# Performance work log

Measured on AMD Instinct MI355X. Metric: run time of the kernel, lower is better.

The kernel has to match this reference:

```python
import jax, jax.numpy as jnp
import numpy as np

N_HEADS = 16
ROPE_BASE = 10000.0

def apply_rope(x):
    # x: [B, H, S, D] with D even; interleaved-pair RoPE (torchtune style)
    B, H, S, D = x.shape
    half = D // 2
    inv_freq = 1.0 / (ROPE_BASE ** (jnp.arange(0, half, dtype=jnp.float32) / half))
    angles = jnp.arange(S, dtype=jnp.float32)[:, None] * inv_freq[None, :]  # [S, D/2]
    cos = jnp.cos(angles)[None, None]  # [1,1,S,D/2]
    sin = jnp.sin(angles)[None, None]
    x1 = x[..., 0::2]
    x2 = x[..., 1::2]
    r1 = x1 * cos - x2 * sin
    r2 = x1 * sin + x2 * cos
    return jnp.stack([r1, r2], axis=-1).reshape(B, H, S, D)

def setup_inputs() -> dict:
    key = jax.random.key(0)
    ks = jax.random.split(key, 5)
    B, S, E = 2, 2048, 1024
    d_attn = 1024
    scale = 1.0 / np.sqrt(E)
    x = jax.random.normal(ks[0], (B, S, E), dtype=jnp.float32)
    Wq = jax.random.normal(ks[1], (d_attn, E), dtype=jnp.float32) * scale
    Wk = jax.random.normal(ks[2], (d_attn, E), dtype=jnp.float32) * scale
    Wv = jax.random.normal(ks[3], (d_attn, E), dtype=jnp.float32) * scale
    Wo = jax.random.normal(ks[4], (E, d_attn), dtype=jnp.float32) * scale
    return {"x": x, "Wq": Wq, "Wk": Wk, "Wv": Wv, "Wo": Wo}

def reference(x, Wq, Wk, Wv, Wo):
    B, S, E = x.shape
    d_attn = Wq.shape[0]
    hd = d_attn // N_HEADS
    attn_scale = 1.0 / np.sqrt(d_attn)
    # projections (nn.Linear: x @ W.T), split heads -> [B, H, S, hd]
    q = (x @ Wq.T).reshape(B, S, N_HEADS, hd).transpose(0, 2, 1, 3)
    k = (x @ Wk.T).reshape(B, S, N_HEADS, hd).transpose(0, 2, 1, 3)
    v = (x @ Wv.T).reshape(B, S, N_HEADS, hd).transpose(0, 2, 1, 3)
    q = apply_rope(q)
    k = apply_rope(k)
    scores = jnp.einsum('bhqd,bhkd->bhqk', q, k) * attn_scale  # [B,H,S,S]
    causal = jnp.tril(jnp.ones((S, S), dtype=bool))
    scores = jnp.where(causal[None, None], scores, -jnp.inf)
    probs = jax.nn.softmax(scores, axis=-1)  # dropout is identity in eval
    out = jnp.einsum('bhqk,bhkd->bhqd', probs, v)
    out = out.transpose(0, 2, 1, 3).reshape(B, S, d_attn)
    return out @ Wo.T
```

## Files before the change

kernel.cpp:

```cpp
#include <hip/hip_runtime.h>


typedef float  f32x4  __attribute__((ext_vector_type(4)));
typedef short  short8 __attribute__((ext_vector_type(8)));

#define MFMA16(a,b,c) __builtin_amdgcn_mfma_f32_16x16x32_bf16((a),(b),(c),0,0,0)
#define GLD_LDS16(g, l)                                                        \
  __builtin_amdgcn_global_load_lds(                                            \
      (const __attribute__((address_space(1))) unsigned int*)(g),              \
      (__attribute__((address_space(3))) unsigned int*)(l), 16, 0, 0)

__device__ __forceinline__ unsigned short f2bf(float f) {
  unsigned int x = __float_as_uint(f);
  x += 0x7fffu + ((x >> 16) & 1u);
  return (unsigned short)(x >> 16);
}
__device__ __forceinline__ float bf2f(unsigned short u) {
  return __uint_as_float(((unsigned int)u) << 16);
}
__device__ __forceinline__ unsigned int cvtpk_bf16(float lo, float hi) {
  unsigned int r;
  asm("v_cvt_pk_bf16_f32 %0, %1, %2" : "=v"(r) : "v"(lo), "v"(hi));
  return r;
}

__global__ __launch_bounds__(256) void cvt_all(const float* __restrict__ x,
                                               const float* __restrict__ wq,
                                               const float* __restrict__ wk,
                                               const float* __restrict__ wv,
                                               const float* __restrict__ wo,
                                               ushort* __restrict__ dst) {
  const int i = blockIdx.x * 256 + threadIdx.x;
  const float* src;
  int off;
  if (i < 1048576) { src = x; off = i; }
  else {
    const int j = i - 1048576;
    const int wsel = j >> 18;
    off = j & 262143;
    src = (wsel == 0) ? wq : (wsel == 1) ? wk : (wsel == 2) ? wv : wo;
  }
  const float4 v = ((const float4*)src)[off];
  ushort4 o = make_ushort4(f2bf(v.x), f2bf(v.y), f2bf(v.z), f2bf(v.w));
  ((ushort4*)dst)[i] = o;
}

template<int MODE, int BN, int BM>
__global__ __launch_bounds__(256) void gemm_bt(const ushort* __restrict__ A,
                                               const ushort* __restrict__ B,
                                               void* __restrict__ Cv,
                                               int K) {
  constexpr int NI = BN / 32;
  constexpr int MI = BM / 32;
  constexpr int AI = BM / 64;
  constexpr int BI = BN / 64;
  __shared__ __align__(16) short As0[BM * 32];
  __shared__ __align__(16) short As1[BM * 32];
  __shared__ __align__(16) short Bs0[BN * 32];
  __shared__ __align__(16) short Bs1[BN * 32];
  const int tid  = threadIdx.x;
  const int lane = tid & 63, w = tid >> 6;
  const int ln   = lane & 15, quad = lane >> 4;
  const int wm   = w >> 1, wn = w & 1;
  const int m0 = blockIdx.y * BM, n0 = blockIdx.x * BN;

  const int srow = lane >> 2;
  const int schk = (lane & 3) * 8;
  const int arow = w * (16 * AI);
  const int brow = w * (16 * BI);
  const ushort* Ag0 = A + (size_t)(m0 + arow + srow) * K + schk;
  const ushort* Ag1 = A + (size_t)(m0 + arow + 16 + srow) * K + schk;
  const ushort* Bg0 = B + (size_t)(n0 + brow + srow) * K + schk;
  const ushort* Bg1 = B + (size_t)(n0 + brow + 16 + srow) * K + schk;
  const int lA0 = arow * 32, lA1 = (arow + 16) * 32;
  const int lB0 = brow * 32, lB1 = (brow + 16) * 32;

  int aoff[MI], boff[NI];
#pragma unroll
  for (int i = 0; i < MI; i++)
    aoff[i] = (wm * (BM / 2) + i * 16 + ln) * 32 + quad * 8;
#pragma unroll
  for (int i = 0; i < NI; i++)
    boff[i] = (wn * (BN / 2) + i * 16 + ln) * 32 + quad * 8;
  f32x4 acc[MI][NI] = {};

  for (int kt = 0; kt < K; kt += 64) {
    __syncthreads();
    GLD_LDS16(Ag0 + kt, As0 + lA0);
    if (AI == 2) GLD_LDS16(Ag1 + kt, As0 + lA1);
    GLD_LDS16(Ag0 + kt + 32, As1 + lA0);
    if (AI == 2) GLD_LDS16(Ag1 + kt + 32, As1 + lA1);
    GLD_LDS16(Bg0 + kt, Bs0 + lB0);
    if (BI == 2) GLD_LDS16(Bg1 + kt, Bs0 + lB1);
    GLD_LDS16(Bg0 + kt + 32, Bs1 + lB0);
    if (BI == 2) GLD_LDS16(Bg1 + kt + 32, Bs1 + lB1);
    __syncthreads();
#pragma unroll
    for (int h = 0; h < 2; ++h) {
      const short* Ap = h ? As1 : As0;
      const short* Bp = h ? Bs1 : Bs0;
      short8 av[MI], bv[NI];
#pragma unroll
      for (int i = 0; i < MI; i++) av[i] = *(const short8*)&Ap[aoff[i]];
#pragma unroll
      for (int i = 0; i < NI; i++) bv[i] = *(const short8*)&Bp[boff[i]];
#pragma unroll
      for (int mi = 0; mi < MI; mi++)
#pragma unroll
        for (int ni = 0; ni < NI; ni++)
          acc[mi][ni] = MFMA16(av[mi], bv[ni], acc[mi][ni]);
    }
  }

  if (MODE == 0) {
    ushort* Cq = (ushort*)Cv;
    if (n0 < 2048) {
      ushort* dst = Cq + (n0 < 1024 ? 0 : 4194304);
      const int nbase = (n0 < 1024) ? n0 : n0 - 1024;
      const float qsc = (n0 < 1024) ? 0.04508422002778011f : 1.0f;
      const float sgn = (ln & 1) ? 1.0f : -1.0f;
      float invc[NI];
#pragma unroll
      for (int ni = 0; ni < NI; ni++) {
        const int ii = ((wn * (BN / 2) + ni * 16 + ln) & 63) >> 1;
        invc[ni] = __builtin_amdgcn_exp2f(-(float)ii * 0.4152410118579865f) *
                   0.15915494309189535f;
      }
#pragma unroll
      for (int mi = 0; mi < MI; mi++) {
        const int row = m0 + wm * (BM / 2) + mi * 16 + quad * 4;
#pragma unroll
        for (int ni = 0; ni < NI; ni++) {
          const int col = nbase + wn * (BN / 2) + ni * 16 + ln;
#pragma unroll
          for (int r = 0; r < 4; r++) {
            const float mine  = acc[mi][ni][r];
            const float other = __shfl_xor(mine, 1, 64);
            const int   s     = (row + r) & 2047;
            const float rev   = (float)s * invc[ni];
            const float rr    = rev - floorf(rev);
            const float sn = __builtin_amdgcn_sinf(rr);
            const float cs = __builtin_amdgcn_cosf(rr);
            const float rot = (mine * cs + sgn * other * sn) * qsc;
            dst[(size_t)(row + r) * 1024 + col] = f2bf(rot);
          }
        }
      }
    } else {
      ushort* vt = Cq + 8388608;
#pragma unroll
      for (int mi = 0; mi < MI; mi++) {
        const int sm = m0 + wm * (BM / 2) + mi * 16 + quad * 4;
        const int b = sm >> 11, s = sm & 2047;
#pragma unroll
        for (int ni = 0; ni < NI; ni++) {
          const int nv = (n0 - 2048) + wn * (BN / 2) + ni * 16 + ln;
          const int bh = b * 16 + (nv >> 6), d = nv & 63;
          ushort4 u = make_ushort4(f2bf(acc[mi][ni][0]), f2bf(acc[mi][ni][1]),
                                   f2bf(acc[mi][ni][2]), f2bf(acc[mi][ni][3]));
          *(ushort4*)&vt[((size_t)bh * 64 + d) * 2048 + s] = u;
        }
      }
    }
  } else {
    float* C = (float*)Cv;
#pragma unroll
    for (int mi = 0; mi < MI; mi++) {
      const int row = m0 + wm * (BM / 2) + mi * 16 + quad * 4;
#pragma unroll
      for (int ni = 0; ni < NI; ni++) {
        const int col = n0 + wn * (BN / 2) + ni * 16 + ln;
#pragma unroll
        for (int r = 0; r < 4; r++)
          C[(size_t)(row + r) * 1024 + col] = acc[mi][ni][r];
      }
    }
  }
}

__global__ __launch_bounds__(512) void attnk(const ushort* __restrict__ q,
                                             const ushort* __restrict__ k,
                                             const ushort* __restrict__ vt,
                                             ushort* __restrict__ ctx) {
  __shared__ __align__(16) short Ks[2][64 * 72];
  __shared__ __align__(16) short Vs[2][64 * 72];
  __shared__ __align__(16) short Ps[8 * 16 * 72];
  const int tid  = threadIdx.x;
  const int lane = tid & 63, w = tid >> 6;
  const int ln   = lane & 15, quad = lane >> 4;
  const int x = blockIdx.x, bh = blockIdx.y;
  const int b = bh >> 4, h = bh & 15;
  const int jA = x, jB = 31 - x;
  const int tile = w >> 2;
  const int wq   = w & 3;
  const int j    = tile ? jA : jB;
  short* Pw = Ps + w * 1152;

  const size_t qb = ((size_t)(b * 2048 + j * 64 + wq * 16 + ln)) * 1024 + h * 64;
  const short8 aq0 = *(const short8*)&q[qb + quad * 8];
  const short8 aq1 = *(const short8*)&q[qb + 32 + quad * 8];

  f32x4 o[4] = {};
  float ls0 = 0.f, ls1 = 0.f;

  const int r0 = tid >> 3, c0 = (tid & 7) * 8;
  const ushort* kg = k  + ((size_t)(b * 2048 + r0)) * 1024 + h * 64 + c0;
  const ushort* vg = vt + ((size_t)(bh * 64 + r0)) * 2048 + c0;
  const int wK = r0 * 72 + c0;

  short8 kr = *(const short8*)(kg);
  short8 vr = *(const short8*)(vg);
  *(short8*)&Ks[0][wK] = kr;
  *(short8*)&Vs[0][wK] = vr;
  kr = *(const short8*)(kg + 65536);
  vr = *(const short8*)(vg + 64);

  const int qloc = j * 64 + wq * 16 + ln;

  for (int t = 0; t <= jB; t++) {
    __syncthreads();
    const short* Kc = Ks[t & 1];
    const short* Vc = Vs[t & 1];
    if (t < jB) {
      *(short8*)&Ks[(t & 1) ^ 1][wK] = kr;
      *(short8*)&Vs[(t & 1) ^ 1][wK] = vr;
    }
    if (t + 2 <= jB) {
      kr = *(const short8*)(kg + (size_t)(t + 2) * 65536);
      vr = *(const short8*)(vg + (t + 2) * 64);
    }

    const bool act = (tile == 0) || (t <= jA);
    if (act) {
      f32x4 sc[4];
#pragma unroll
      for (int ct = 0; ct < 4; ct++) {
        const short8 bk0 = *(const short8*)&Kc[(ct * 16 + ln) * 72 + quad * 8];
        const short8 bk1 = *(const short8*)&Kc[(ct * 16 + ln) * 72 + 32 + quad * 8];
        f32x4 z = {0.f, 0.f, 0.f, 0.f};
        z = MFMA16(bk0, aq0, z);
        z = MFMA16(bk1, aq1, z);
        sc[ct] = z;
      }
      if (t == j) {
#pragma unroll
        for (int ct = 0; ct < 4; ct++) {
          const int kvb = (t << 6) + ct * 16 + quad * 4;
#pragma unroll
          for (int r = 0; r < 4; r++)
            if (kvb + r > qloc) sc[ct][r] = -100000.0f;
        }
      }

      short8 bv0[4], bv1[4];
#pragma unroll
      for (int dt = 0; dt < 4; dt++) {
        bv0[dt] = *(const short8*)&Vc[(dt * 16 + ln) * 72 + quad * 8];
        bv1[dt] = *(const short8*)&Vc[(dt * 16 + ln) * 72 + 32 + quad * 8];
      }

#pragma unroll
      for (int ct = 0; ct < 4; ct++) {
        const float p0 = __builtin_amdgcn_exp2f(sc[ct][0]);
        const float p1 = __builtin_amdgcn_exp2f(sc[ct][1]);
        const float p2 = __builtin_amdgcn_exp2f(sc[ct][2]);
        const float p3 = __builtin_amdgcn_exp2f(sc[ct][3]);
        ls0 += p0 + p1;
        ls1 += p2 + p3;
        const uint2 u = make_uint2(cvtpk_bf16(p0, p1), cvtpk_bf16(p2, p3));
        *(uint2*)&Pw[ln * 72 + ct * 16 + quad * 4] = u;
      }
      const short8 ap0 = *(const short8*)&Pw[ln * 72 + quad * 8];
      const short8 ap1 = *(const short8*)&Pw[ln * 72 + 32 + quad * 8];
#pragma unroll
      for (int dt = 0; dt < 4; dt++) {
        o[dt] = MFMA16(ap0, bv0[dt], o[dt]);
        o[dt] = MFMA16(ap1, bv1[dt], o[dt]);
      }
    }
  }

  float l = ls0 + ls1;
  l += __shfl_xor(l, 16, 64);
  l += __shfl_xor(l, 32, 64);

#pragma unroll
  for (int r = 0; r < 4; r++) {
    const float inv = 1.0f / __shfl(l, quad * 4 + r, 64);
    const int row = j * 64 + wq * 16 + quad * 4 + r;
#pragma unroll
    for (int dt = 0; dt < 4; dt++) {
      ctx[((size_t)(b * 2048 + row)) * 1024 + h * 64 + dt * 16 + ln] =
          f2bf(o[dt][r] * inv);
    }
  }
}

extern "C" void kernel_launch(void* const* d_in, const int* in_sizes, int n_in,
                              void* d_out, int out_size, void* d_ws, size_t ws_size,
                              hipStream_t stream) {
  const float* x  = (const float*)d_in[0];
  const float* Wq = (const float*)d_in[1];
  const float* Wk = (const float*)d_in[2];
  const float* Wv = (const float*)d_in[3];
  const float* Wo = (const float*)d_in[4];
  float* out = (float*)d_out;
  char* ws = (char*)d_ws;

  ushort* xb  = (ushort*)(ws);
  ushort* wqb = (ushort*)(ws + (size_t)(8  << 20));
  ushort* qb  = (ushort*)(ws + (size_t)(16 << 20));
  ushort* kb  = (ushort*)(ws + (size_t)(24 << 20));
  ushort* vtb = (ushort*)(ws + (size_t)(32 << 20));
  ushort* ctx = (ushort*)(ws + (size_t)(40 << 20));

  cvt_all<<<8192, 256, 0, stream>>>(x, Wq, Wk, Wv, Wo, xb);
  gemm_bt<0, 64, 128><<<dim3(48, 32), 256, 0, stream>>>(xb, wqb, (void*)qb, 1024);
  attnk<<<dim3(16, 32), 512, 0, stream>>>(qb, kb, vtb, ctx);
  gemm_bt<2, 64, 64><<<dim3(16, 64), 256, 0, stream>>>(ctx, wqb + 3145728 , (void*)out, 1024);
}
```

Measured before the change: 175.1 us.

## Split attention KV tiles across wave groups instead of query tiles for balance

Previously the two wave groups each handled one of the paired query tiles (jA, jB), so the jA group went idle once its shorter causal range ended. Now both groups work on both query tiles and split each 64-key KV tile in half (32 keys each). Partial outputs and row sums are combined through shared memory at the end. This keeps all waves busy for the whole loop, at the cost of a final reduction, extra barriers and more registers for two accumulator sets.

```diff
diff --git a/kernel.cpp b/kernel.cpp
--- a/kernel.cpp
+++ b/kernel.cpp
@@ -184,24 +184,29 @@
                                              ushort* __restrict__ ctx) {
   __shared__ __align__(16) short Ks[2][64 * 72];
   __shared__ __align__(16) short Vs[2][64 * 72];
-  __shared__ __align__(16) short Ps[8 * 16 * 72];
+  __shared__ __align__(16) short PsB[8][16 * 48];
+  __shared__ __align__(16) short PsA[8][16 * 48];
   const int tid  = threadIdx.x;
   const int lane = tid & 63, w = tid >> 6;
   const int ln   = lane & 15, quad = lane >> 4;
   const int x = blockIdx.x, bh = blockIdx.y;
   const int b = bh >> 4, h = bh & 15;
   const int jA = x, jB = 31 - x;
-  const int tile = w >> 2;
+  const int g    = w >> 2;
   const int wq   = w & 3;
-  const int j    = tile ? jA : jB;
-  short* Pw = Ps + w * 1152;
-
-  const size_t qb = ((size_t)(b * 2048 + j * 64 + wq * 16 + ln)) * 1024 + h * 64;
-  const short8 aq0 = *(const short8*)&q[qb + quad * 8];
-  const short8 aq1 = *(const short8*)&q[qb + 32 + quad * 8];
-
-  f32x4 o[4] = {};
-  float ls0 = 0.f, ls1 = 0.f;
+  const int koff = g * 32;
+  short* PwB = PsB[w];
+  short* PwA = PsA[w];
+
+  const size_t qbA = ((size_t)(b * 2048 + jA * 64 + wq * 16 + ln)) * 1024 + h * 64;
+  const size_t qbB = ((size_t)(b * 2048 + jB * 64 + wq * 16 + ln)) * 1024 + h * 64;
+  const short8 aqA0 = *(const short8*)&q[qbA + quad * 8];
+  const short8 aqA1 = *(const short8*)&q[qbA + 32 + quad * 8];
+  const short8 aqB0 = *(const short8*)&q[qbB + quad * 8];
+  const short8 aqB1 = *(const short8*)&q[qbB + 32 + quad * 8];
+
+  f32x4 oA[4] = {}, oB[4] = {};
+  float lsA0 = 0.f, lsA1 = 0.f, lsB0 = 0.f, lsB1 = 0.f;
 
   const int r0 = tid >> 3, c0 = (tid & 7) * 8;
   const ushort* kg = k  + ((size_t)(b * 2048 + r0)) * 1024 + h * 64 + c0;
@@ -215,7 +220,8 @@
   kr = *(const short8*)(kg + 65536);
   vr = *(const short8*)(vg + 64);
 
-  const int qloc = j * 64 + wq * 16 + ln;
+  const int qlocA = jA * 64 + wq * 16 + ln;
+  const int qlocB = jB * 64 + wq * 16 + ln;
 
   for (int t = 0; t <= jB; t++) {
     __syncthreads();
@@ -230,68 +236,132 @@
       vr = *(const short8*)(vg + (t + 2) * 64);
     }
 
-    const bool act = (tile == 0) || (t <= jA);
-    if (act) {
-      f32x4 sc[4];
-#pragma unroll
-      for (int ct = 0; ct < 4; ct++) {
-        const short8 bk0 = *(const short8*)&Kc[(ct * 16 + ln) * 72 + quad * 8];
-        const short8 bk1 = *(const short8*)&Kc[(ct * 16 + ln) * 72 + 32 + quad * 8];
-        f32x4 z = {0.f, 0.f, 0.f, 0.f};
-        z = MFMA16(bk0, aq0, z);
-        z = MFMA16(bk1, aq1, z);
-        sc[ct] = z;
-      }
-      if (t == j) {
-#pragma unroll
-        for (int ct = 0; ct < 4; ct++) {
-          const int kvb = (t << 6) + ct * 16 + quad * 4;
-#pragma unroll
-          for (int r = 0; r < 4; r++)
-            if (kvb + r > qloc) sc[ct][r] = -100000.0f;
-        }
-      }
-
-      short8 bv0[4], bv1[4];
+    const bool actA = (t <= jA);
+    f32x4 scB[2], scA[2];
+#pragma unroll
+    for (int c = 0; c < 2; c++) {
+      const int ct = 2 * g + c;
+      const short8 bk0 = *(const short8*)&Kc[(ct * 16 + ln) * 72 + quad * 8];
+      const short8 bk1 = *(const short8*)&Kc[(ct * 16 + ln) * 72 + 32 + quad * 8];
+      f32x4 z = {0.f, 0.f, 0.f, 0.f};
+      z = MFMA16(bk0, aqB0, z);
+      z = MFMA16(bk1, aqB1, z);
+      scB[c] = z;
+      if (actA) {
+        f32x4 y = {0.f, 0.f, 0.f, 0.f};
+        y = MFMA16(bk0, aqA0, y);
+        y = MFMA16(bk1, aqA1, y);
+        scA[c] = y;
+      }
+    }
+    if (t == jB) {
+#pragma unroll
+      for (int c = 0; c < 2; c++) {
+        const int kvb = (t << 6) + (2 * g + c) * 16 + quad * 4;
+#pragma unroll
+        for (int r = 0; r < 4; r++)
+          if (kvb + r > qlocB) scB[c][r] = -100000.0f;
+      }
+    }
+    if (actA && t == jA) {
+#pragma unroll
+      for (int c = 0; c < 2; c++) {
+        const int kvb = (t << 6) + (2 * g + c) * 16 + quad * 4;
+#pragma unroll
+        for (int r = 0; r < 4; r++)
+          if (kvb + r > qlocA) scA[c][r] = -100000.0f;
+      }
+    }
+
+    short8 bv[4];
+#pragma unroll
+    for (int dt = 0; dt < 4; dt++)
+      bv[dt] = *(const short8*)&Vc[(dt * 16 + ln) * 72 + koff + quad * 8];
+
+#pragma unroll
+    for (int c = 0; c < 2; c++) {
+      const float p0 = __builtin_amdgcn_exp2f(scB[c][0]);
+      const float p1 = __builtin_amdgcn_exp2f(scB[c][1]);
+      const float p2 = __builtin_amdgcn_exp2f(scB[c][2]);
+      const float p3 = __builtin_amdgcn_exp2f(scB[c][3]);
+      lsB0 += p0 + p1;
+      lsB1 += p2 + p3;
+      const uint2 u = make_uint2(cvtpk_bf16(p0, p1), cvtpk_bf16(p2, p3));
+      *(uint2*)&PwB[ln * 48 + c * 16 + quad * 4] = u;
+    }
+    {
+      const short8 ap = *(const short8*)&PwB[ln * 48 + quad * 8];
+#pragma unroll
+      for (int dt = 0; dt < 4; dt++)
+        oB[dt] = MFMA16(ap, bv[dt], oB[dt]);
+    }
+    if (actA) {
+#pragma unroll
+      for (int c = 0; c < 2; c++) {
+        const float p0 = __builtin_amdgcn_exp2f(scA[c][0]);
+        const float p1 = __builtin_amdgcn_exp2f(scA[c][1]);
+        const float p2 = __builtin_amdgcn_exp2f(scA[c][2]);
+        const float p3 = __builtin_amdgcn_exp2f(scA[c][3]);
+        lsA0 += p0 + p1;
+        lsA1 += p2 + p3;
+        const uint2 u = make_uint2(cvtpk_bf16(p0, p1), cvtpk_bf16(p2, p3));
+        *(uint2*)&PwA[ln * 48 + c * 16 + quad * 4] = u;
+      }
+      const short8 ap = *(const short8*)&PwA[ln * 48 + quad * 8];
+#pragma unroll
+      for (int dt = 0; dt < 4; dt++)
+        oA[dt] = MFMA16(ap, bv[dt], oA[dt]);
+    }
+  }
+
+  float lA = lsA0 + lsA1, lB = lsB0 + lsB1;
+  lA += __shfl_xor(lA, 16, 64);
+  lA += __shfl_xor(lA, 32, 64);
+  lB += __shfl_xor(lB, 16, 64);
+  lB += __shfl_xor(lB, 32, 64);
+
+  __syncthreads();
+  if (g == 1) {
+    float* dB = (float*)Ks + ((wq * 64 + lane) * 16);
+    float* dA = (float*)Vs + ((wq * 64 + lane) * 16);
+#pragma unroll
+    for (int dt = 0; dt < 4; dt++)
+#pragma unroll
+      for (int r = 0; r < 4; r++) {
+        dB[dt * 4 + r] = oB[dt][r];
+        dA[dt * 4 + r] = oA[dt][r];
+      }
+    float* dl = (float*)PsB + (wq * 64 + lane) * 2;
+    dl[0] = lB;
+    dl[1] = lA;
+  }
+  __syncthreads();
+  if (g == 0) {
+    const float* sB = (const float*)Ks + ((wq * 64 + lane) * 16);
+    const float* sA = (const float*)Vs + ((wq * 64 + lane) * 16);
+    const float* sl = (const float*)PsB + (wq * 64 + lane) * 2;
+    lB += sl[0];
+    lA += sl[1];
+#pragma unroll
+    for (int dt = 0; dt < 4; dt++)
+#pragma unroll
+      for (int r = 0; r < 4; r++) {
+        oB[dt][r] += sB[dt * 4 + r];
+        oA[dt][r] += sA[dt * 4 + r];
+      }
+#pragma unroll
+    for (int r = 0; r < 4; r++) {
+      const float invB = 1.0f / __shfl(lB, quad * 4 + r, 64);
+      const float invA = 1.0f / __shfl(lA, quad * 4 + r, 64);
+      const int rowB = jB * 64 + wq * 16 + quad * 4 + r;
+      const int rowA = jA * 64 + wq * 16 + quad * 4 + r;
 #pragma unroll
       for (int dt = 0; dt < 4; dt++) {
-        bv0[dt] = *(const short8*)&Vc[(dt * 16 + ln) * 72 + quad * 8];
-        bv1[dt] = *(const short8*)&Vc[(dt * 16 + ln) * 72 + 32 + quad * 8];
-      }
-
-#pragma unroll
-      for (int ct = 0; ct < 4; ct++) {
-        const float p0 = __builtin_amdgcn_exp2f(sc[ct][0]);
-        const float p1 = __builtin_amdgcn_exp2f(sc[ct][1]);
-        const float p2 = __builtin_amdgcn_exp2f(sc[ct][2]);
-        const float p3 = __builtin_amdgcn_exp2f(sc[ct][3]);
-        ls0 += p0 + p1;
-        ls1 += p2 + p3;
-        const uint2 u = make_uint2(cvtpk_bf16(p0, p1), cvtpk_bf16(p2, p3));
-        *(uint2*)&Pw[ln * 72 + ct * 16 + quad * 4] = u;
-      }
-      const short8 ap0 = *(const short8*)&Pw[ln * 72 + quad * 8];
-      const short8 ap1 = *(const short8*)&Pw[ln * 72 + 32 + quad * 8];
-#pragma unroll
-      for (int dt = 0; dt < 4; dt++) {
-        o[dt] = MFMA16(ap0, bv0[dt], o[dt]);
-        o[dt] = MFMA16(ap1, bv1[dt], o[dt]);
-      }
-    }
-  }
-
-  float l = ls0 + ls1;
-  l += __shfl_xor(l, 16, 64);
-  l += __shfl_xor(l, 32, 64);
-
-#pragma unroll
-  for (int r = 0; r < 4; r++) {
-    const float inv = 1.0f / __shfl(l, quad * 4 + r, 64);
-    const int row = j * 64 + wq * 16 + quad * 4 + r;
-#pragma unroll
-    for (int dt = 0; dt < 4; dt++) {
-      ctx[((size_t)(b * 2048 + row)) * 1024 + h * 64 + dt * 16 + ln] =
-          f2bf(o[dt][r] * inv);
+        ctx[((size_t)(b * 2048 + rowB)) * 1024 + h * 64 + dt * 16 + ln] =
+            f2bf(oB[dt][r] * invB);
+        ctx[((size_t)(b * 2048 + rowA)) * 1024 + h * 64 + dt * 16 + ln] =
+            f2bf(oA[dt][r] * invA);
+      }
     }
   }
 }
```

Measured after the change: 177.0 us. No clear change (+1.1%).
